# Performance work log

Measured on AMD Instinct MI355X. Metric: run time of the kernel, lower is better.

## Reference

```python
import jax, jax.numpy as jnp
import numpy as np

BAG = 15          # bag_size
STEPS = 5
LAM = 1e-3        # anti_hebb_lambda
PS = 8            # patch_size
IM = 28           # image_size
DEN = IM - PS     # position normalization denominator (=20)
KEEP = 0.1        # 1 - recurrent_sparsity


def _ln(h, gamma, beta, eps=1e-5):
    mu = jnp.mean(h, axis=-1, keepdims=True)
    var = jnp.mean((h - mu) ** 2, axis=-1, keepdims=True)
    return (h - mu) * jax.lax.rsqrt(var + eps) * gamma + beta


def _patch(img, pos):
    # img: [IM, IM], pos: [2] int32 -> flattened PSxPS patch [PS*PS]
    return jax.lax.dynamic_slice(img, (pos[0], pos[1]), (PS, PS)).reshape(PS * PS)

_extract = jax.vmap(_patch)  # [B,IM,IM], [B,2] -> [B, PS*PS]


def setup_inputs() -> dict:
    key = jax.random.key(0)
    ks = jax.random.split(key, 8)
    B = 65536
    x = jax.random.normal(ks[0], (B, 1, IM, IM), jnp.float32)
    in_dim = PS * PS + 2
    Wi = jax.random.normal(ks[1], (BAG, in_dim), jnp.float32) * np.sqrt(2.0 / in_dim)
    bi = jnp.zeros((BAG,), jnp.float32)
    gamma = jnp.ones((BAG,), jnp.float32)
    beta = jnp.zeros((BAG,), jnp.float32)
    mask = (jax.random.uniform(ks[2], (BAG, BAG)) < KEEP).astype(jnp.float32)
    R = jax.random.normal(ks[3], (BAG, BAG), jnp.float32) * np.sqrt(2.0 / BAG) * mask
    rb = jnp.zeros((BAG,), jnp.float32)
    Wc = jax.random.normal(ks[4], (2, BAG), jnp.float32) * np.sqrt(2.0 / BAG)
    bc = jnp.zeros((2,), jnp.float32)
    Wo = jax.random.normal(ks[5], (10, BAG), jnp.float32) * np.sqrt(2.0 / BAG)
    bo = jnp.zeros((10,), jnp.float32)
    return dict(x=x, Wi=Wi, bi=bi, gamma=gamma, beta=beta, R=R, rb=rb,
                mask=mask, Wc=Wc, bc=bc, Wo=Wo, bo=bo)


def reference(x, Wi, bi, gamma, beta, R, rb, mask, Wc, bc, Wo, bo):
    B = x.shape[0]
    imgs = x[:, 0]  # [B, IM, IM]
    positions = jnp.full((B, 2), (IM - PS) // 2, dtype=jnp.int32)
    state = None
    logits = None
    for _ in range(STEPS):  # small fixed step count; state/positions recur
        flat = _extract(imgs, positions)                       # [B, 64]
        pos = positions.astype(x.dtype) / DEN * 2.0 - 1.0      # [B, 2]
        in_act = jnp.concatenate([flat, pos], axis=1) @ Wi.T + bi
        if state is None:
            state = _ln(jax.nn.relu(in_act), gamma, beta)
        else:
            coact = jnp.einsum('bi,bj->ij', state, state) / B  # [BAG, BAG]
            Reff = (R - LAM * coact) * mask
            state = _ln(jax.nn.relu(in_act + state @ Reff.T + rb), gamma, beta)
        logits = state @ Wo.T + bo                             # [B, 10]
        ctrl = jnp.tanh(state @ Wc.T + bc)                     # [B, 2]
        mag_r = jnp.abs(ctrl[:, 0])
        mag_c = jnp.abs(ctrl[:, 1])
        row_sel = mag_r >= mag_c
        row_move = jnp.where(row_sel, jnp.sign(ctrl[:, 0]).astype(jnp.int32), 0)
        col_move = jnp.where(row_sel, 0, jnp.sign(ctrl[:, 1]).astype(jnp.int32))
        positions = jnp.clip(positions + jnp.stack([row_move, col_move], axis=1), 0, IM - PS)
    return logits
```

## Files before the change

### kernel.cpp

```cpp
#include <hip/hip_runtime.h>
#include <math.h>

#define IMSZ 28
#define PSZ  8
#define LAMF 0.001f
#define NREP 8
#define CSTRIDE 240

template<bool FIRST, bool LAST>
__global__ __launch_bounds__(256, 8) void step8(
    const float* __restrict__ x,
    const float* __restrict__ Wi, const float* __restrict__ bi,
    const float* __restrict__ gamma, const float* __restrict__ beta,
    const float* __restrict__ R, const float* __restrict__ rb,
    const float* __restrict__ mask,
    const float* __restrict__ Wc, const float* __restrict__ bc,
    const float* __restrict__ Wo, const float* __restrict__ bo,
    float* __restrict__ state, int* __restrict__ pos,
    const float* __restrict__ coact_in, float* __restrict__ coact_out,
    float* __restrict__ out, int B, float invB)
{
    __shared__ float sWi[15 * 72];
    __shared__ float sBi[16], sGa[16], sBe[16], sRb[16];
    __shared__ float sWc[32], sBc[2], sWo[160], sBo[16];
    __shared__ float sReff[240];
    __shared__ float sS[32 * 16];

    const int tid = threadIdx.x;

    for (int idx = tid; idx < 990; idx += 256) {
        int u = idx / 66, k = idx - u * 66;
        sWi[u * 72 + k] = Wi[idx];
    }
    if (tid < 15) {
        sBi[tid] = bi[tid]; sGa[tid] = gamma[tid];
        sBe[tid] = beta[tid]; sRb[tid] = rb[tid];
    }
    if (tid >= 32 && tid < 62) sWc[tid - 32] = Wc[tid - 32];
    if (tid >= 64 && tid < 66) sBc[tid - 64] = bc[tid - 64];
    if (LAST) {
        if (tid >= 96 && tid < 246) sWo[tid - 96] = Wo[tid - 96];
        if (tid >= 246) sBo[tid - 246] = bo[tid - 246];
    }
    if (!FIRST) {
        if (tid < 225) {
            float cv = 0.0f;
#pragma unroll
            for (int r = 0; r < NREP; ++r) cv += coact_in[r * CSTRIDE + tid];
            sReff[tid] = (R[tid] - LAMF * (cv * invB)) * mask[tid];
        } else if (tid < 240) {
            sReff[tid] = 0.0f;
        }
    }
    __syncthreads();

    const int sib = tid >> 3;
    const int row = tid & 7;
    const int b = blockIdx.x * 32 + sib;

    int pr, pc;
    if (FIRST) { pr = 10; pc = 10; }
    else { int p = pos[b]; pr = p >> 8; pc = p & 255; }

    const float* rowp = x + (size_t)b * (IMSZ * IMSZ) + (pr + row) * IMSZ + pc;
    float patch[8];
#pragma unroll
    for (int c = 0; c < 8; ++c) patch[c] = rowp[c];

    const float posr = ((float)pr / 20.0f) * 2.0f - 1.0f;
    const float posc = ((float)pc / 20.0f) * 2.0f - 1.0f;

    float sj0 = 0.0f, sj1 = 0.0f;
    if (!FIRST) {
        sj0 = state[b * 16 + row];
        sj1 = (row < 7) ? state[b * 16 + 8 + row] : 0.0f;
    }

    float h[15];
#pragma unroll
    for (int u = 0; u < 15; ++u) {
        const float* w = sWi + u * 72 + row * 8;
        float a = 0.0f;
#pragma unroll
        for (int c = 0; c < 8; ++c) a = fmaf(patch[c], w[c], a);
        if (!FIRST) {
            a = fmaf(sj0, sReff[u * 15 + row], a);
            a = fmaf(sj1, sReff[u * 15 + 8 + row], a);
        }
        if (row == 0) {
            a = fmaf(posr, sWi[u * 72 + 64], a);
            a = fmaf(posc, sWi[u * 72 + 65], a);
            a += sBi[u];
            if (!FIRST) a += sRb[u];
        }
        h[u] = a;
    }

#pragma unroll
    for (int u = 0; u < 15; ++u) {
        float v = h[u];
        v += __shfl_xor(v, 1);
        v += __shfl_xor(v, 2);
        v += __shfl_xor(v, 4);
        h[u] = fmaxf(v, 0.0f);
    }

    float mu = 0.0f;
#pragma unroll
    for (int u = 0; u < 15; ++u) mu += h[u];
    mu *= (1.0f / 15.0f);
    float var = 0.0f;
#pragma unroll
    for (int u = 0; u < 15; ++u) { float d = h[u] - mu; var = fmaf(d, d, var); }
    var *= (1.0f / 15.0f);
    const float rs = 1.0f / sqrtf(var + 1e-5f);
    float st[15];
#pragma unroll
    for (int u = 0; u < 15; ++u) st[u] = (h[u] - mu) * rs * sGa[u] + sBe[u];

    if (LAST) {
#pragma unroll
        for (int rep = 0; rep < 2; ++rep) {
            int o = rep * 8 + row;
            if (o < 10) {
                float a = 0.0f;
#pragma unroll
                for (int j = 0; j < 15; ++j) a = fmaf(st[j], sWo[o * 15 + j], a);
                out[(size_t)b * 10 + o] = a + sBo[o];
            }
        }
    } else {
        state[b * 16 + row] = st[row];
        if (row < 7) state[b * 16 + 8 + row] = st[8 + row];

        float c0 = 0.0f, c1 = 0.0f;
#pragma unroll
        for (int j = 0; j < 15; ++j) {
            c0 = fmaf(st[j], sWc[j], c0);
            c1 = fmaf(st[j], sWc[15 + j], c1);
        }
        c0 = tanhf(c0 + sBc[0]);
        c1 = tanhf(c1 + sBc[1]);
        const float m0 = fabsf(c0), m1 = fabsf(c1);
        int rm, cm;
        if (m0 >= m1) { rm = (c0 > 0.0f) - (c0 < 0.0f); cm = 0; }
        else          { rm = 0; cm = (c1 > 0.0f) - (c1 < 0.0f); }
        pr = min(max(pr + rm, 0), IMSZ - PSZ);
        pc = min(max(pc + cm, 0), IMSZ - PSZ);
        if (row == 0) pos[b] = (pr << 8) | pc;

        sS[sib * 16 + row] = st[row];
        if (row < 7) sS[sib * 16 + 8 + row] = st[8 + row];
        __syncthreads();
        if (tid < 225) {
            int i = tid / 15, j = tid - i * 15;
            float acc = 0.0f;
#pragma unroll
            for (int bb = 0; bb < 32; ++bb)
                acc = fmaf(sS[bb * 16 + i], sS[bb * 16 + j], acc);
            atomicAdd(&coact_out[(blockIdx.x & (NREP - 1)) * CSTRIDE + tid], acc);
        }
    }
}

extern "C" void kernel_launch(void* const* d_in, const int* in_sizes, int n_in,
                              void* d_out, int out_size, void* d_ws, size_t ws_size,
                              hipStream_t stream) {
    const float* x     = (const float*)d_in[0];
    const float* Wi    = (const float*)d_in[1];
    const float* bi    = (const float*)d_in[2];
    const float* gamma = (const float*)d_in[3];
    const float* beta  = (const float*)d_in[4];
    const float* R     = (const float*)d_in[5];
    const float* rb    = (const float*)d_in[6];
    const float* mask  = (const float*)d_in[7];
    const float* Wc    = (const float*)d_in[8];
    const float* bc    = (const float*)d_in[9];
    const float* Wo    = (const float*)d_in[10];
    const float* bo    = (const float*)d_in[11];
    float* out = (float*)d_out;

    const int B = in_sizes[0] / (IMSZ * IMSZ);
    const float invB = 1.0f / (float)B;
    const int grid = B / 32;

    float* wsf = (float*)d_ws;
    float* state = wsf;
    int* pos = (int*)(wsf + (size_t)B * 16);
    float* coact = wsf + (size_t)B * 16 + (size_t)B;

    hipMemsetAsync(coact, 0, (size_t)4 * NREP * CSTRIDE * sizeof(float), stream);

    step8<true, false><<<grid, 256, 0, stream>>>(
        x, Wi, bi, gamma, beta, R, rb, mask, Wc, bc, Wo, bo,
        state, pos, nullptr, coact + 0 * NREP * CSTRIDE, nullptr, B, invB);
    step8<false, false><<<grid, 256, 0, stream>>>(
        x, Wi, bi, gamma, beta, R, rb, mask, Wc, bc, Wo, bo,
        state, pos, coact + 0 * NREP * CSTRIDE, coact + 1 * NREP * CSTRIDE, nullptr, B, invB);
    step8<false, false><<<grid, 256, 0, stream>>>(
        x, Wi, bi, gamma, beta, R, rb, mask, Wc, bc, Wo, bo,
        state, pos, coact + 1 * NREP * CSTRIDE, coact + 2 * NREP * CSTRIDE, nullptr, B, invB);
    step8<false, false><<<grid, 256, 0, stream>>>(
        x, Wi, bi, gamma, beta, R, rb, mask, Wc, bc, Wo, bo,
        state, pos, coact + 2 * NREP * CSTRIDE, coact + 3 * NREP * CSTRIDE, nullptr, B, invB);
    step8<false, true><<<grid, 256, 0, stream>>>(
        x, Wi, bi, gamma, beta, R, rb, mask, Wc, bc, Wo, bo,
        state, pos, coact + 3 * NREP * CSTRIDE, nullptr, out, B, invB);
}
```

Before: 354.3 us.

## Fuse five step kernels into one persistent kernel with grid-wide barriers

Replaces five separate step launches with a single kernel. Each 1024-thread block handles 256 samples for all five steps and keeps state and positions in registers and shared memory instead of global workspace. A software grid barrier (atomic counter plus spin) separates steps so the global coactivation sums are complete before the next step reads them. It also transposes the patch mapping so each lane reads a column, and doubles the replica count for the coact atomics. This removes launch gaps and state/pos round trips. The cost is 256 blocks spinning on barriers, and the kernel relies on all blocks being co-resident or it will deadlock.

```diff
diff --git a/kernel.cpp b/kernel.cpp
--- a/kernel.cpp
+++ b/kernel.cpp
@@ -4,11 +4,11 @@
 #define IMSZ 28
 #define PSZ  8
 #define LAMF 0.001f
-#define NREP 8
+#define NREP 16
 #define CSTRIDE 240
-
-template<bool FIRST, bool LAST>
-__global__ __launch_bounds__(256, 8) void step8(
+#define SSTR 17
+
+__global__ __launch_bounds__(1024, 4) void fused5(
     const float* __restrict__ x,
     const float* __restrict__ Wi, const float* __restrict__ bi,
     const float* __restrict__ gamma, const float* __restrict__ beta,
@@ -16,19 +16,19 @@
     const float* __restrict__ mask,
     const float* __restrict__ Wc, const float* __restrict__ bc,
     const float* __restrict__ Wo, const float* __restrict__ bo,
-    float* __restrict__ state, int* __restrict__ pos,
-    const float* __restrict__ coact_in, float* __restrict__ coact_out,
-    float* __restrict__ out, int B, float invB)
+    float* __restrict__ coact, unsigned* __restrict__ bar,
+    float* __restrict__ out, float invB, int nblk)
 {
     __shared__ float sWi[15 * 72];
     __shared__ float sBi[16], sGa[16], sBe[16], sRb[16];
     __shared__ float sWc[32], sBc[2], sWo[160], sBo[16];
+    __shared__ float sRm[226], sLm[226];
     __shared__ float sReff[240];
-    __shared__ float sS[32 * 16];
+    __shared__ float sS[256 * SSTR];
 
     const int tid = threadIdx.x;
 
-    for (int idx = tid; idx < 990; idx += 256) {
+    for (int idx = tid; idx < 990; idx += 1024) {
         int u = idx / 66, k = idx - u * 66;
         sWi[u * 72 + k] = Wi[idx];
     }
@@ -36,129 +36,204 @@
         sBi[tid] = bi[tid]; sGa[tid] = gamma[tid];
         sBe[tid] = beta[tid]; sRb[tid] = rb[tid];
     }
-    if (tid >= 32 && tid < 62) sWc[tid - 32] = Wc[tid - 32];
-    if (tid >= 64 && tid < 66) sBc[tid - 64] = bc[tid - 64];
-    if (LAST) {
-        if (tid >= 96 && tid < 246) sWo[tid - 96] = Wo[tid - 96];
-        if (tid >= 246) sBo[tid - 246] = bo[tid - 246];
-    }
-    if (!FIRST) {
-        if (tid < 225) {
-            float cv = 0.0f;
-#pragma unroll
-            for (int r = 0; r < NREP; ++r) cv += coact_in[r * CSTRIDE + tid];
-            sReff[tid] = (R[tid] - LAMF * (cv * invB)) * mask[tid];
-        } else if (tid < 240) {
-            sReff[tid] = 0.0f;
-        }
-    }
+    if (tid >= 32 && tid < 62)  sWc[tid - 32] = Wc[tid - 32];
+    if (tid >= 62 && tid < 64)  sBc[tid - 62] = bc[tid - 62];
+    if (tid >= 96 && tid < 246) sWo[tid - 96] = Wo[tid - 96];
+    if (tid >= 246 && tid < 256) sBo[tid - 246] = bo[tid - 246];
+    if (tid >= 256 && tid < 481) {
+        int t = tid - 256;
+        float m = mask[t];
+        sRm[t] = R[t] * m;
+        sLm[t] = (LAMF * invB) * m;
+    }
+    if (tid >= 481 && tid < 496) sReff[tid - 256] = 0.0f;
     __syncthreads();
 
-    const int sib = tid >> 3;
-    const int row = tid & 7;
-    const int b = blockIdx.x * 32 + sib;
-
-    int pr, pc;
-    if (FIRST) { pr = 10; pc = 10; }
-    else { int p = pos[b]; pr = p >> 8; pc = p & 255; }
-
-    const float* rowp = x + (size_t)b * (IMSZ * IMSZ) + (pr + row) * IMSZ + pc;
-    float patch[8];
-#pragma unroll
-    for (int c = 0; c < 8; ++c) patch[c] = rowp[c];
-
-    const float posr = ((float)pr / 20.0f) * 2.0f - 1.0f;
-    const float posc = ((float)pc / 20.0f) * 2.0f - 1.0f;
-
-    float sj0 = 0.0f, sj1 = 0.0f;
-    if (!FIRST) {
-        sj0 = state[b * 16 + row];
-        sj1 = (row < 7) ? state[b * 16 + 8 + row] : 0.0f;
-    }
-
-    float h[15];
-#pragma unroll
-    for (int u = 0; u < 15; ++u) {
-        const float* w = sWi + u * 72 + row * 8;
-        float a = 0.0f;
-#pragma unroll
-        for (int c = 0; c < 8; ++c) a = fmaf(patch[c], w[c], a);
-        if (!FIRST) {
-            a = fmaf(sj0, sReff[u * 15 + row], a);
-            a = fmaf(sj1, sReff[u * 15 + 8 + row], a);
-        }
-        if (row == 0) {
-            a = fmaf(posr, sWi[u * 72 + 64], a);
-            a = fmaf(posc, sWi[u * 72 + 65], a);
-            a += sBi[u];
-            if (!FIRST) a += sRb[u];
-        }
-        h[u] = a;
-    }
-
-#pragma unroll
-    for (int u = 0; u < 15; ++u) {
-        float v = h[u];
-        v += __shfl_xor(v, 1);
-        v += __shfl_xor(v, 2);
-        v += __shfl_xor(v, 4);
-        h[u] = fmaxf(v, 0.0f);
-    }
-
-    float mu = 0.0f;
-#pragma unroll
-    for (int u = 0; u < 15; ++u) mu += h[u];
-    mu *= (1.0f / 15.0f);
-    float var = 0.0f;
-#pragma unroll
-    for (int u = 0; u < 15; ++u) { float d = h[u] - mu; var = fmaf(d, d, var); }
-    var *= (1.0f / 15.0f);
-    const float rs = 1.0f / sqrtf(var + 1e-5f);
-    float st[15];
-#pragma unroll
-    for (int u = 0; u < 15; ++u) st[u] = (h[u] - mu) * rs * sGa[u] + sBe[u];
-
-    if (LAST) {
-#pragma unroll
-        for (int rep = 0; rep < 2; ++rep) {
-            int o = rep * 8 + row;
-            if (o < 10) {
-                float a = 0.0f;
-#pragma unroll
-                for (int j = 0; j < 15; ++j) a = fmaf(st[j], sWo[o * 15 + j], a);
-                out[(size_t)b * 10 + o] = a + sBo[o];
-            }
-        }
-    } else {
-        state[b * 16 + row] = st[row];
-        if (row < 7) state[b * 16 + 8 + row] = st[8 + row];
-
-        float c0 = 0.0f, c1 = 0.0f;
-#pragma unroll
-        for (int j = 0; j < 15; ++j) {
-            c0 = fmaf(st[j], sWc[j], c0);
-            c1 = fmaf(st[j], sWc[15 + j], c1);
-        }
-        c0 = tanhf(c0 + sBc[0]);
-        c1 = tanhf(c1 + sBc[1]);
-        const float m0 = fabsf(c0), m1 = fabsf(c1);
-        int rm, cm;
-        if (m0 >= m1) { rm = (c0 > 0.0f) - (c0 < 0.0f); cm = 0; }
-        else          { rm = 0; cm = (c1 > 0.0f) - (c1 < 0.0f); }
-        pr = min(max(pr + rm, 0), IMSZ - PSZ);
-        pc = min(max(pc + cm, 0), IMSZ - PSZ);
-        if (row == 0) pos[b] = (pr << 8) | pc;
-
-        sS[sib * 16 + row] = st[row];
-        if (row < 7) sS[sib * 16 + 8 + row] = st[8 + row];
-        __syncthreads();
-        if (tid < 225) {
-            int i = tid / 15, j = tid - i * 15;
-            float acc = 0.0f;
-#pragma unroll
-            for (int bb = 0; bb < 32; ++bb)
-                acc = fmaf(sS[bb * 16 + i], sS[bb * 16 + j], acc);
-            atomicAdd(&coact_out[(blockIdx.x & (NREP - 1)) * CSTRIDE + tid], acc);
+    const int g = tid >> 3;
+    const int c = tid & 7;
+    const int b0 = blockIdx.x * 256 + g;
+    const int b1 = b0 + 128;
+    const float* img0 = x + (size_t)b0 * (IMSZ * IMSZ);
+    const float* img1 = x + (size_t)b1 * (IMSZ * IMSZ);
+
+    int pr0 = 10, pc0 = 10, pr1 = 10, pc1 = 10;
+    float hA[15], hB[15];
+
+    for (int s = 0; s < 5; ++s) {
+        float sj0A = 0.f, sj1A = 0.f, sj0B = 0.f, sj1B = 0.f;
+        if (s > 0) {
+            sj0A = sS[g * SSTR + c];
+            sj0B = sS[(g + 128) * SSTR + c];
+            if (c < 7) {
+                sj1A = sS[g * SSTR + 8 + c];
+                sj1B = sS[(g + 128) * SSTR + 8 + c];
+            }
+            if (tid < 225) {
+                const float* ci = coact + (size_t)(s - 1) * (NREP * CSTRIDE) + tid;
+                float cv = 0.0f;
+#pragma unroll
+                for (int r = 0; r < NREP; ++r)
+                    cv += __hip_atomic_load(ci + (size_t)r * CSTRIDE,
+                                            __ATOMIC_RELAXED, __HIP_MEMORY_SCOPE_AGENT);
+                sReff[tid] = sRm[tid] - sLm[tid] * cv;
+            }
+            __syncthreads();
+        }
+
+        float pA[8], pB[8];
+        {
+            const float* q0 = img0 + pr0 * IMSZ + pc0 + c;
+            const float* q1 = img1 + pr1 * IMSZ + pc1 + c;
+#pragma unroll
+            for (int r = 0; r < 8; ++r) { pA[r] = q0[r * IMSZ]; pB[r] = q1[r * IMSZ]; }
+        }
+
+        const float fr0 = ((float)pr0 / 20.0f) * 2.0f - 1.0f;
+        const float fc0 = ((float)pc0 / 20.0f) * 2.0f - 1.0f;
+        const float fr1 = ((float)pr1 / 20.0f) * 2.0f - 1.0f;
+        const float fc1 = ((float)pc1 / 20.0f) * 2.0f - 1.0f;
+
+#pragma unroll
+        for (int u = 0; u < 15; ++u) {
+            float a = 0.f, bq = 0.f;
+            const float* w = sWi + u * 72 + c;
+#pragma unroll
+            for (int r = 0; r < 8; ++r) {
+                float wv = w[r * 8];
+                a  = fmaf(pA[r], wv, a);
+                bq = fmaf(pB[r], wv, bq);
+            }
+            if (s > 0) {
+                float w0 = sReff[u * 15 + c];
+                float w1 = sReff[u * 15 + 8 + c];
+                a  = fmaf(sj0A, w0, a);  a  = fmaf(sj1A, w1, a);
+                bq = fmaf(sj0B, w0, bq); bq = fmaf(sj1B, w1, bq);
+            }
+            if (c == 0) {
+                float wr = sWi[u * 72 + 64], wc = sWi[u * 72 + 65];
+                float bias = sBi[u] + ((s > 0) ? sRb[u] : 0.0f);
+                a  = fmaf(fr0, wr, a);  a  = fmaf(fc0, wc, a);  a  += bias;
+                bq = fmaf(fr1, wr, bq); bq = fmaf(fc1, wc, bq); bq += bias;
+            }
+            hA[u] = a; hB[u] = bq;
+        }
+
+#pragma unroll
+        for (int u = 0; u < 15; ++u) {
+            float vA = hA[u], vB = hB[u];
+            vA += __shfl_xor(vA, 1); vB += __shfl_xor(vB, 1);
+            vA += __shfl_xor(vA, 2); vB += __shfl_xor(vB, 2);
+            vA += __shfl_xor(vA, 4); vB += __shfl_xor(vB, 4);
+            hA[u] = fmaxf(vA, 0.0f);
+            hB[u] = fmaxf(vB, 0.0f);
+        }
+
+        float muA = 0.f, muB = 0.f;
+#pragma unroll
+        for (int u = 0; u < 15; ++u) { muA += hA[u]; muB += hB[u]; }
+        muA *= (1.0f / 15.0f); muB *= (1.0f / 15.0f);
+        float vA = 0.f, vB = 0.f;
+#pragma unroll
+        for (int u = 0; u < 15; ++u) {
+            float dA = hA[u] - muA; vA = fmaf(dA, dA, vA);
+            float dB = hB[u] - muB; vB = fmaf(dB, dB, vB);
+        }
+        vA *= (1.0f / 15.0f); vB *= (1.0f / 15.0f);
+        const float rsA = 1.0f / sqrtf(vA + 1e-5f);
+        const float rsB = 1.0f / sqrtf(vB + 1e-5f);
+#pragma unroll
+        for (int u = 0; u < 15; ++u) {
+            hA[u] = (hA[u] - muA) * rsA * sGa[u] + sBe[u];
+            hB[u] = (hB[u] - muB) * rsB * sGa[u] + sBe[u];
+        }
+
+        if (s == 4) {
+#pragma unroll
+            for (int rep = 0; rep < 2; ++rep) {
+                int o = rep * 8 + c;
+                if (o < 10) {
+                    float a0 = 0.f, a1 = 0.f;
+#pragma unroll
+                    for (int j = 0; j < 15; ++j) {
+                        a0 = fmaf(hA[j], sWo[o * 15 + j], a0);
+                        a1 = fmaf(hB[j], sWo[o * 15 + j], a1);
+                    }
+                    out[(size_t)b0 * 10 + o] = a0 + sBo[o];
+                    out[(size_t)b1 * 10 + o] = a1 + sBo[o];
+                }
+            }
+        } else {
+            float c0A = 0.f, c1A = 0.f, c0B = 0.f, c1B = 0.f;
+#pragma unroll
+            for (int j = 0; j < 15; ++j) {
+                c0A = fmaf(hA[j], sWc[j],      c0A);
+                c1A = fmaf(hA[j], sWc[15 + j], c1A);
+                c0B = fmaf(hB[j], sWc[j],      c0B);
+                c1B = fmaf(hB[j], sWc[15 + j], c1B);
+            }
+            c0A = tanhf(c0A + sBc[0]); c1A = tanhf(c1A + sBc[1]);
+            c0B = tanhf(c0B + sBc[0]); c1B = tanhf(c1B + sBc[1]);
+            {
+                float m0 = fabsf(c0A), m1 = fabsf(c1A);
+                int rm, cm;
+                if (m0 >= m1) { rm = (c0A > 0.f) - (c0A < 0.f); cm = 0; }
+                else          { rm = 0; cm = (c1A > 0.f) - (c1A < 0.f); }
+                pr0 = min(max(pr0 + rm, 0), IMSZ - PSZ);
+                pc0 = min(max(pc0 + cm, 0), IMSZ - PSZ);
+            }
+            {
+                float m0 = fabsf(c0B), m1 = fabsf(c1B);
+                int rm, cm;
+                if (m0 >= m1) { rm = (c0B > 0.f) - (c0B < 0.f); cm = 0; }
+                else          { rm = 0; cm = (c1B > 0.f) - (c1B < 0.f); }
+                pr1 = min(max(pr1 + rm, 0), IMSZ - PSZ);
+                pc1 = min(max(pc1 + cm, 0), IMSZ - PSZ);
+            }
+
+#pragma unroll
+            for (int k = 0; k < 8; ++k) {
+                if (c == k) {
+                    sS[g * SSTR + k]         = hA[k];
+                    sS[(g + 128) * SSTR + k] = hB[k];
+                    if (k < 7) {
+                        sS[g * SSTR + 8 + k]         = hA[8 + k];
+                        sS[(g + 128) * SSTR + 8 + k] = hB[8 + k];
+                    }
+                }
+            }
+            __syncthreads();
+
+            {
+                const int q = tid >> 8;
+                const int t = tid & 255;
+                if (t < 225) {
+                    int i = t / 15, j = t - i * 15;
+                    const int base = q * 64;
+                    float a0 = 0.f, a1 = 0.f, a2 = 0.f, a3 = 0.f;
+#pragma unroll
+                    for (int bb = 0; bb < 64; bb += 4) {
+                        a0 = fmaf(sS[(base + bb + 0) * SSTR + i], sS[(base + bb + 0) * SSTR + j], a0);
+                        a1 = fmaf(sS[(base + bb + 1) * SSTR + i], sS[(base + bb + 1) * SSTR + j], a1);
+                        a2 = fmaf(sS[(base + bb + 2) * SSTR + i], sS[(base + bb + 2) * SSTR + j], a2);
+                        a3 = fmaf(sS[(base + bb + 3) * SSTR + i], sS[(base + bb + 3) * SSTR + j], a3);
+                    }
+                    atomicAdd(&coact[(size_t)s * (NREP * CSTRIDE)
+                                     + ((blockIdx.x * 4 + q) & (NREP - 1)) * CSTRIDE + t],
+                              (a0 + a1) + (a2 + a3));
+                }
+            }
+
+            __threadfence();
+            __syncthreads();
+            if (tid == 0) {
+                __hip_atomic_fetch_add(&bar[s * 16], 1u,
+                                       __ATOMIC_ACQ_REL, __HIP_MEMORY_SCOPE_AGENT);
+                while (__hip_atomic_load(&bar[s * 16],
+                                         __ATOMIC_ACQUIRE, __HIP_MEMORY_SCOPE_AGENT)
+                       < (unsigned)nblk)
+                    __builtin_amdgcn_s_sleep(2);
+            }
+            __syncthreads();
         }
     }
 }
@@ -166,6 +241,7 @@
 extern "C" void kernel_launch(void* const* d_in, const int* in_sizes, int n_in,
                               void* d_out, int out_size, void* d_ws, size_t ws_size,
                               hipStream_t stream) {
+    (void)n_in; (void)out_size; (void)ws_size;
     const float* x     = (const float*)d_in[0];
     const float* Wi    = (const float*)d_in[1];
     const float* bi    = (const float*)d_in[2];
@@ -182,28 +258,16 @@
 
     const int B = in_sizes[0] / (IMSZ * IMSZ);
     const float invB = 1.0f / (float)B;
-    const int grid = B / 32;
-
-    float* wsf = (float*)d_ws;
-    float* state = wsf;
-    int* pos = (int*)(wsf + (size_t)B * 16);
-    float* coact = wsf + (size_t)B * 16 + (size_t)B;
-
-    hipMemsetAsync(coact, 0, (size_t)4 * NREP * CSTRIDE * sizeof(float), stream);
-
-    step8<true, false><<<grid, 256, 0, stream>>>(
+    int grid = B / 256;
+
+    float* coact = (float*)d_ws;
+    unsigned* bar = (unsigned*)(coact + 4 * NREP * CSTRIDE);
+
+    hipMemsetAsync(d_ws, 0,
+                   (size_t)4 * NREP * CSTRIDE * sizeof(float) + 16 * 16 * sizeof(unsigned),
+                   stream);
+
+    fused5<<<grid, 1024, 0, stream>>>(
         x, Wi, bi, gamma, beta, R, rb, mask, Wc, bc, Wo, bo,
-        state, pos, nullptr, coact + 0 * NREP * CSTRIDE, nullptr, B, invB);
-    step8<false, false><<<grid, 256, 0, stream>>>(
-        x, Wi, bi, gamma, beta, R, rb, mask, Wc, bc, Wo, bo,
-        state, pos, coact + 0 * NREP * CSTRIDE, coact + 1 * NREP * CSTRIDE, nullptr, B, invB);
-    step8<false, false><<<grid, 256, 0, stream>>>(
-        x, Wi, bi, gamma, beta, R, rb, mask, Wc, bc, Wo, bo,
-        state, pos, coact + 1 * NREP * CSTRIDE, coact + 2 * NREP * CSTRIDE, nullptr, B, invB);
-    step8<false, false><<<grid, 256, 0, stream>>>(
-        x, Wi, bi, gamma, beta, R, rb, mask, Wc, bc, Wo, bo,
-        state, pos, coact + 2 * NREP * CSTRIDE, coact + 3 * NREP * CSTRIDE, nullptr, B, invB);
-    step8<false, true><<<grid, 256, 0, stream>>>(
-        x, Wi, bi, gamma, beta, R, rb, mask, Wc, bc, Wo, bo,
-        state, pos, coact + 3 * NREP * CSTRIDE, nullptr, out, B, invB);
+        coact, bar, out, invB, grid);
 }
```

Result: slower. 625.5 us (+76.6%).
